# Performance work log

Measured on AMD Instinct MI355X. Metric: run time of the kernel, lower is better.

Reference implementation:

```python
import jax, jax.numpy as jnp
import numpy as np

LEAK = 0.2

def setup_inputs() -> dict:
    key = jax.random.key(0)
    ks = jax.random.split(key, 8)
    B, D, H1, H2, F = 2048, 3072, 512, 256, 100
    s = lambda fan_in: 1.0 / np.sqrt(fan_in)
    return {
        "x":  jax.random.normal(ks[0], (B, D), dtype=jnp.float32),
        "W1": jax.random.uniform(ks[1], (D, H1), jnp.float32, -s(D), s(D)),
        "b1": jnp.zeros((H1,), jnp.float32),
        "W2": jax.random.uniform(ks[2], (H1, H2), jnp.float32, -s(H1), s(H1)),
        "b2": jnp.zeros((H2,), jnp.float32),
        "T":  jax.random.normal(ks[3], (H2, F), dtype=jnp.float32),
        "Wf": jax.random.uniform(ks[4], (H2 + F, 1), jnp.float32, -s(H2 + F), s(H2 + F)),
        "bf": jnp.zeros((1,), jnp.float32),
    }

def reference(x, W1, b1, W2, b2, T, Wf, bf):
    # MLP stack with LeakyReLU(0.2)
    h = jax.nn.leaky_relu(x @ W1 + b1, LEAK)          # (B,512)
    h = jax.nn.leaky_relu(h @ W2 + b2, LEAK)          # (B,256)
    # Minibatch discrimination: pairwise L1 per feature, exp, sum over batch
    m = h @ T                                          # (B,100)
    d = jnp.abs(m[:, None, :] - m[None, :, :])         # (B,B,100)
    feats = jnp.sum(jnp.exp(-d), axis=1)               # (B,100)
    z = jnp.concatenate([h, feats], axis=1)            # (B,356)
    return z @ Wf + bf                                 # (B,1)
```

## Files before the change

### kernel.cpp

```cpp
#include <hip/hip_runtime.h>
#include <hip/hip_bf16.h>

#define LEAK 0.2f

typedef __attribute__((ext_vector_type(8))) short short8;
typedef __attribute__((ext_vector_type(4))) float f32x4;


__global__ __launch_bounds__(256) void k_prep(const float* __restrict__ x,
                                              __hip_bfloat16* __restrict__ xb,
                                              const float* __restrict__ W1,
                                              __hip_bfloat16* __restrict__ W1t,
                                              const float* __restrict__ W2,
                                              __hip_bfloat16* __restrict__ W2t,
                                              const float* __restrict__ T,
                                              __hip_bfloat16* __restrict__ Tt) {
  int b = blockIdx.x;
  int t = threadIdx.x;
  if (b < 6144) {
    int idx = b * 256 + t;
    float4 v = reinterpret_cast<const float4*>(x)[idx];
    union { ushort4 u; __hip_bfloat16 h[4]; } c;
    c.h[0] = __float2bfloat16(v.x);
    c.h[1] = __float2bfloat16(v.y);
    c.h[2] = __float2bfloat16(v.z);
    c.h[3] = __float2bfloat16(v.w);
    reinterpret_cast<ushort4*>(xb)[idx] = c.u;
    return;
  }
  __shared__ float tile[32][33];
  const float* W;
  __hip_bfloat16* Wt;
  int K, N, kblk, nblk;
  int b2 = b - 6144;
  if (b2 < 1536) {
    W = W1; Wt = W1t; K = 3072; N = 512;
    kblk = b2 % 96; nblk = b2 / 96;
  } else if (b2 < 1664) {
    int b3 = b2 - 1536;
    W = W2; Wt = W2t; K = 512; N = 256;
    kblk = b3 % 16; nblk = b3 / 16;
  } else {
    int b4 = b2 - 1664;
    W = T; Wt = Tt; K = 256; N = 100;
    kblk = b4 % 8; nblk = b4 / 8;
  }
  int k0 = kblk * 32, n0 = nblk * 32;
  int tx = t & 31, ty = t >> 5;
#pragma unroll
  for (int r = 0; r < 4; ++r) {
    int n = n0 + tx;
    tile[ty + r * 8][tx] = (n < N) ? W[(long)(k0 + ty + r * 8) * N + n] : 0.f;
  }
  __syncthreads();
#pragma unroll
  for (int r = 0; r < 4; ++r)
    Wt[(long)(n0 + ty + r * 8) * K + k0 + tx] = __float2bfloat16(tile[tx][ty + r * 8]);
}

template <bool TRANSP, bool BF16OUT>
__global__ __launch_bounds__(256) void k_gemm(const __hip_bfloat16* __restrict__ A,
                                              const __hip_bfloat16* __restrict__ Bt,
                                              float* __restrict__ Cp,
                                              int M, int N, int K, int KSPL, int ldO) {
  __shared__ __align__(16) __hip_bfloat16 As[64][72];
  __shared__ __align__(16) __hip_bfloat16 Bs[64][72];
  int tid = threadIdx.x;
  int lane = tid & 63;
  int wv = tid >> 6;
  int wm = wv & 1, wn = wv >> 1;
  int quad = lane >> 4, l16 = lane & 15;
  long m0 = (long)blockIdx.x * 64, n0 = (long)blockIdx.y * 64;
  int srow = tid >> 2, scol = (tid & 3) * 16;
  int kStart = blockIdx.z * KSPL;
  const __hip_bfloat16* Ag = A + (m0 + srow) * K + kStart + scol;
  const __hip_bfloat16* Bg = Bt + (n0 + srow) * K + kStart + scol;

  int4 ra0 = *reinterpret_cast<const int4*>(Ag);
  int4 ra1 = *reinterpret_cast<const int4*>(Ag + 8);
  int4 rb0 = *reinterpret_cast<const int4*>(Bg);
  int4 rb1 = *reinterpret_cast<const int4*>(Bg + 8);

  f32x4 acc[2][2] = {};
  for (int kb = 0; kb < KSPL; kb += 64) {
    *reinterpret_cast<int4*>(&As[srow][scol]) = ra0;
    *reinterpret_cast<int4*>(&As[srow][scol + 8]) = ra1;
    *reinterpret_cast<int4*>(&Bs[srow][scol]) = rb0;
    *reinterpret_cast<int4*>(&Bs[srow][scol + 8]) = rb1;
    __syncthreads();
    if (kb + 64 < KSPL) {
      ra0 = *reinterpret_cast<const int4*>(Ag + kb + 64);
      ra1 = *reinterpret_cast<const int4*>(Ag + kb + 72);
      rb0 = *reinterpret_cast<const int4*>(Bg + kb + 64);
      rb1 = *reinterpret_cast<const int4*>(Bg + kb + 72);
    }
#pragma unroll
    for (int half = 0; half < 2; ++half) {
      short8 af[2], bfr[2];
#pragma unroll
      for (int t = 0; t < 2; ++t) {
        af[t]  = *reinterpret_cast<const short8*>(&As[wm * 32 + t * 16 + l16][half * 32 + quad * 8]);
        bfr[t] = *reinterpret_cast<const short8*>(&Bs[wn * 32 + t * 16 + l16][half * 32 + quad * 8]);
      }
#pragma unroll
      for (int tm = 0; tm < 2; ++tm)
#pragma unroll
        for (int tn = 0; tn < 2; ++tn)
          acc[tm][tn] =
              __builtin_amdgcn_mfma_f32_16x16x32_bf16(af[tm], bfr[tn], acc[tm][tn], 0, 0, 0);
    }
    __syncthreads();
  }

#pragma unroll
  for (int tm = 0; tm < 2; ++tm)
#pragma unroll
    for (int tn = 0; tn < 2; ++tn)
#pragma unroll
      for (int r = 0; r < 4; ++r) {
        long gm = m0 + wm * 32 + tm * 16 + quad * 4 + r;
        long gn = n0 + wn * 32 + tn * 16 + l16;
        long off = TRANSP ? (gn * ldO + gm) : (gm * ldO + gn);
        if constexpr (BF16OUT) {
          __hip_bfloat16* Cz = reinterpret_cast<__hip_bfloat16*>(Cp) + (long)blockIdx.z * M * N;
          Cz[off] = __float2bfloat16(acc[tm][tn][r]);
        } else {
          float* Cz = Cp + (long)blockIdx.z * M * N;
          Cz[off] = acc[tm][tn][r];
        }
      }
}

template <int NZ>
__global__ __launch_bounds__(256) void k_comb_bf(const __hip_bfloat16* __restrict__ P,
                                                 const float* __restrict__ bias,
                                                 __hip_bfloat16* __restrict__ Ob,
                                                 int total8, int nmask) {
  int idx = blockIdx.x * 256 + threadIdx.x;
  if (idx >= total8) return;
  union u8 { short8 v; ushort u[8]; };
  u8 z[NZ], o;
#pragma unroll
  for (int q = 0; q < NZ; ++q)
    z[q].v = reinterpret_cast<const short8*>(P + (long)q * total8 * 8)[idx];
  int col = (idx * 8) & nmask;
  float4 b0 = *reinterpret_cast<const float4*>(bias + col);
  float4 b1 = *reinterpret_cast<const float4*>(bias + col + 4);
  float bs[8] = {b0.x, b0.y, b0.z, b0.w, b1.x, b1.y, b1.z, b1.w};
#pragma unroll
  for (int j = 0; j < 8; ++j) {
    float v = bs[j];
#pragma unroll
    for (int q = 0; q < NZ; ++q) {
      union { ushort u; __hip_bfloat16 h; } cc;
      cc.u = z[q].u[j];
      v += __bfloat162float(cc.h);
    }
    v = v > 0.f ? v : LEAK * v;
    union { ushort u; __hip_bfloat16 h; } co;
    co.h = __float2bfloat16(v);
    o.u[j] = co.u;
  }
  reinterpret_cast<short8*>(Ob)[idx] = o.v;
}

__global__ __launch_bounds__(256) void k_comb2row(const float* __restrict__ P,
                                                  const float* __restrict__ bias,
                                                  const float* __restrict__ Wf,
                                                  const float* __restrict__ bfp,
                                                  __hip_bfloat16* __restrict__ h2b,
                                                  float* __restrict__ out) {
  int wv = threadIdx.x >> 6, lane = threadIdx.x & 63;
  long i = (long)blockIdx.x * 4 + wv;
  long off = i * 256 + lane * 4;
  float4 v = *reinterpret_cast<const float4*>(P + off);
  float4 a = *reinterpret_cast<const float4*>(P + 2048L * 256 + off);
  v.x += a.x; v.y += a.y; v.z += a.z; v.w += a.w;
  float4 bs = *reinterpret_cast<const float4*>(bias + lane * 4);
  v.x += bs.x; v.y += bs.y; v.z += bs.z; v.w += bs.w;
  v.x = v.x > 0.f ? v.x : LEAK * v.x;
  v.y = v.y > 0.f ? v.y : LEAK * v.y;
  v.z = v.z > 0.f ? v.z : LEAK * v.z;
  v.w = v.w > 0.f ? v.w : LEAK * v.w;
  union { ushort4 u; __hip_bfloat16 h[4]; } c;
  c.h[0] = __float2bfloat16(v.x);
  c.h[1] = __float2bfloat16(v.y);
  c.h[2] = __float2bfloat16(v.z);
  c.h[3] = __float2bfloat16(v.w);
  reinterpret_cast<ushort4*>(h2b)[i * 64 + lane] = c.u;
  float4 wfv = *reinterpret_cast<const float4*>(Wf + lane * 4);
  float s = v.x * wfv.x + v.y * wfv.y + v.z * wfv.z + v.w * wfv.w;
#pragma unroll
  for (int d = 32; d; d >>= 1) s += __shfl_down(s, d);
  if (lane == 0) out[i] = s + bfp[0];
}

__global__ __launch_bounds__(1024) void k_bucketfeats(const float* __restrict__ mTz,
                                                      float* __restrict__ featsT) {
  __shared__ float sP[2048], sN[2048];
  __shared__ float Sp[2048], Sn[2048];
  __shared__ int Smeta[2048];
  __shared__ short sB[2048];
  __shared__ int cnt[256], bstart[256], bcur[256];
  __shared__ float bsP[256], bsN[256], Pbel[256], Nab[256];
  __shared__ float wred[32];
  __shared__ float sMin, sMax;
  int f = blockIdx.x;
  int t = threadIdx.x;
  int lane = t & 63, wv = t >> 6;
  const long FS = 2048L * 128;
  const float* row = mTz + (long)f * 2048;

  float m[2];
  float lmin = 3.4e38f, lmax = -3.4e38f;
#pragma unroll
  for (int r = 0; r < 2; ++r) {
    int e = t + r * 1024;
    float v = row[e] + row[FS + e] + row[2 * FS + e] + row[3 * FS + e];
    m[r] = v;
    lmin = fminf(lmin, v);
    lmax = fmaxf(lmax, v);
  }
#pragma unroll
  for (int d = 32; d; d >>= 1) {
    lmin = fminf(lmin, __shfl_down(lmin, d));
    lmax = fmaxf(lmax, __shfl_down(lmax, d));
  }
  if (lane == 0) { wred[wv] = lmin; wred[16 + wv] = lmax; }
  if (t < 256) cnt[t] = 0;
  __syncthreads();
  if (t == 0) {
    float a = wred[0], b = wred[16];
    for (int i = 1; i < 16; ++i) { a = fminf(a, wred[i]); b = fmaxf(b, wred[16 + i]); }
    sMin = a; sMax = b;
  }
  __syncthreads();
  float mn = sMin, mx = sMax;
  float rge = mx - mn;
  float scale = (rge > 1e-20f) ? 255.0f / rge : 0.f;
  float mid = 0.5f * (mn + mx);
#pragma unroll
  for (int r = 0; r < 2; ++r) {
    int e = t + r * 1024;
    float v = m[r];
    int b = (int)((v - mn) * scale);
    b = b < 255 ? b : 255;
    float arg = fminf(fmaxf(v - mid, -60.f), 60.f);
    sP[e] = __expf(arg);
    sN[e] = __expf(-arg);
    sB[e] = (short)b;
    atomicAdd(&cnt[b], 1);
  }
  __syncthreads();
  if (wv == 0) {
    int b4 = lane * 4;
    int c0 = cnt[b4], c1 = cnt[b4 + 1], c2 = cnt[b4 + 2], c3 = cnt[b4 + 3];
    int tot = c0 + c1 + c2 + c3;
    int inc = tot;
#pragma unroll
    for (int d = 1; d < 64; d <<= 1) {
      int y = __shfl_up(inc, d);
      if (lane >= d) inc += y;
    }
    int run = inc - tot;
    bstart[b4] = run; bcur[b4] = run; run += c0;
    bstart[b4 + 1] = run; bcur[b4 + 1] = run; run += c1;
    bstart[b4 + 2] = run; bcur[b4 + 2] = run; run += c2;
    bstart[b4 + 3] = run; bcur[b4 + 3] = run;
  }
  __syncthreads();
#pragma unroll
  for (int r = 0; r < 2; ++r) {
    int e = t + r * 1024;
    int b = sB[e];
    int slot = atomicAdd(&bcur[b], 1);
    Sp[slot] = sP[e];
    Sn[slot] = sN[e];
    Smeta[slot] = (b << 16) | e;
  }
  __syncthreads();
  if (t < 256) {
    int s0 = bstart[t], s1 = s0 + cnt[t];
    float ap = 0.f, an = 0.f;
    for (int q = s0; q < s1; ++q) { ap += Sp[q]; an += Sn[q]; }
    bsP[t] = ap; bsN[t] = an;
  }
  __syncthreads();
  if (wv == 0) {
    int b4 = lane * 4;
    float p0 = bsP[b4], p1 = bsP[b4 + 1], p2 = bsP[b4 + 2], p3 = bsP[b4 + 3];
    float n0 = bsN[b4], n1 = bsN[b4 + 1], n2 = bsN[b4 + 2], n3 = bsN[b4 + 3];
    float tp = p0 + p1 + p2 + p3, tn = n0 + n1 + n2 + n3;
    float ip = tp, in_ = tn;
#pragma unroll
    for (int d = 1; d < 64; d <<= 1) {
      float yp = __shfl_up(ip, d);
      float yn = __shfl_up(in_, d);
      if (lane >= d) { ip += yp; in_ += yn; }
    }
    float totn = __shfl(in_, 63);
    float runp = ip - tp;
    float runn = in_ - tn;
    Pbel[b4] = runp; Nab[b4] = totn - runn - n0; runp += p0; runn += n0;
    Pbel[b4 + 1] = runp; Nab[b4 + 1] = totn - runn - n1; runp += p1; runn += n1;
    Pbel[b4 + 2] = runp; Nab[b4 + 2] = totn - runn - n2; runp += p2; runn += n2;
    Pbel[b4 + 3] = runp; Nab[b4 + 3] = totn - runn - n3;
  }
  __syncthreads();
#pragma unroll
  for (int r = 0; r < 2; ++r) {
    int s = t + r * 1024;
    int meta = Smeta[s];
    int b = meta >> 16;
    int idx = meta & 0xFFFF;
    float p = Sp[s], n = Sn[s];
    float acc = n * Pbel[b] + p * Nab[b];
    int q0 = bstart[b], q1 = q0 + cnt[b];
    for (int q = q0; q < q1; ++q) acc += fminf(p * Sn[q], n * Sp[q]);
    featsT[(long)f * 2048 + idx] = acc;
  }
}

__global__ __launch_bounds__(256) void k_final(const float* __restrict__ featsT,
                                               const float* __restrict__ Wf,
                                               float* __restrict__ out) {
  int wv = threadIdx.x >> 6, lane = threadIdx.x & 63;
  long i = (long)blockIdx.x * 4 + wv;
  float s = 0.f;
  for (int f = lane; f < 100; f += 64) s += featsT[(long)f * 2048 + i] * Wf[256 + f];
#pragma unroll
  for (int off = 32; off; off >>= 1) s += __shfl_down(s, off);
  if (lane == 0) out[i] += s;
}

extern "C" void kernel_launch(void* const* d_in, const int* in_sizes, int n_in,
                              void* d_out, int out_size, void* d_ws, size_t ws_size,
                              hipStream_t stream) {
  const float* x  = (const float*)d_in[0];
  const float* W1 = (const float*)d_in[1];
  const float* b1 = (const float*)d_in[2];
  const float* W2 = (const float*)d_in[3];
  const float* b2 = (const float*)d_in[4];
  const float* T  = (const float*)d_in[5];
  const float* Wf = (const float*)d_in[6];
  const float* bf = (const float*)d_in[7];
  float* out = (float*)d_out;

  char* w = (char*)d_ws;
  auto alloc = [&](size_t b) { char* p = w; w += (b + 255) & ~(size_t)255; return p; };
  __hip_bfloat16* xb  = (__hip_bfloat16*)alloc(2048L * 3072 * 2);
  __hip_bfloat16* W1t = (__hip_bfloat16*)alloc(512L * 3072 * 2);
  __hip_bfloat16* W2t = (__hip_bfloat16*)alloc(256L * 512 * 2);
  __hip_bfloat16* Tt  = (__hip_bfloat16*)alloc(128L * 256 * 2);
  __hip_bfloat16* h1b = (__hip_bfloat16*)alloc(2048L * 512 * 2);
  __hip_bfloat16* h2b = (__hip_bfloat16*)alloc(2048L * 256 * 2);
  float*          feT = (float*)alloc(100L * 2048 * 4);
  __hip_bfloat16* P1  = (__hip_bfloat16*)alloc(6L * 2048 * 512 * 2);
  float*          P2  = (float*)alloc(2L * 2048 * 256 * 4);
  float*          P3  = (float*)alloc(4L * 2048 * 128 * 4);

  k_prep<<<7840, 256, 0, stream>>>(x, xb, W1, W1t, W2, W2t, T, Tt);
  k_gemm<false, true><<<dim3(32, 8, 6), 256, 0, stream>>>(xb, W1t, (float*)P1, 2048, 512, 3072, 512, 512);
  k_comb_bf<6><<<512, 256, 0, stream>>>(P1, b1, h1b, 131072, 511);
  k_gemm<false, false><<<dim3(32, 4, 2), 256, 0, stream>>>(h1b, W2t, P2, 2048, 256, 512, 256, 256);
  k_comb2row<<<512, 256, 0, stream>>>(P2, b2, Wf, bf, h2b, out);
  k_gemm<true, false><<<dim3(32, 2, 4), 256, 0, stream>>>(h2b, Tt, P3, 2048, 128, 256, 64, 2048);
  k_bucketfeats<<<100, 1024, 0, stream>>>(P3, feT);
  k_final<<<512, 256, 0, stream>>>(feT, Wf, out);
}
```

Before: 126.9 us.

## Stage transposed GEMM output through LDS, halve split-K, use bf16 partials for layer 2

The transposed-output GEMM now writes its tile to shared memory and stores coalesced float4 rows, replacing scattered strided writes. The first GEMM's split-K count drops from six to three slices, which halves the partial-sum traffic and the reduction work in the combine kernel but leaves fewer blocks to run in parallel. The second GEMM now writes bf16 partials instead of fp32, and the combine kernel reads bf16, trading some accuracy for less memory traffic.

```diff
diff --git a/kernel.cpp b/kernel.cpp
--- a/kernel.cpp
+++ b/kernel.cpp
@@ -63,6 +63,7 @@
                                               const __hip_bfloat16* __restrict__ Bt,
                                               float* __restrict__ Cp,
                                               int M, int N, int K, int KSPL, int ldO) {
+  static_assert(!(TRANSP && BF16OUT), "unused combo");
   __shared__ __align__(16) __hip_bfloat16 As[64][72];
   __shared__ __align__(16) __hip_bfloat16 Bs[64][72];
   int tid = threadIdx.x;
@@ -112,23 +113,46 @@
     __syncthreads();
   }
 
-#pragma unroll
-  for (int tm = 0; tm < 2; ++tm)
-#pragma unroll
-    for (int tn = 0; tn < 2; ++tn)
-#pragma unroll
-      for (int r = 0; r < 4; ++r) {
-        long gm = m0 + wm * 32 + tm * 16 + quad * 4 + r;
-        long gn = n0 + wn * 32 + tn * 16 + l16;
-        long off = TRANSP ? (gn * ldO + gm) : (gm * ldO + gn);
-        if constexpr (BF16OUT) {
-          __hip_bfloat16* Cz = reinterpret_cast<__hip_bfloat16*>(Cp) + (long)blockIdx.z * M * N;
-          Cz[off] = __float2bfloat16(acc[tm][tn][r]);
-        } else {
-          float* Cz = Cp + (long)blockIdx.z * M * N;
-          Cz[off] = acc[tm][tn][r];
+  if constexpr (TRANSP) {
+    __shared__ float Sf[64][65];
+#pragma unroll
+    for (int tm = 0; tm < 2; ++tm)
+#pragma unroll
+      for (int tn = 0; tn < 2; ++tn)
+#pragma unroll
+        for (int r = 0; r < 4; ++r) {
+          int lr = wm * 32 + tm * 16 + quad * 4 + r;
+          int lc = wn * 32 + tn * 16 + l16;
+          Sf[lc][lr] = acc[tm][tn][r];
         }
-      }
+    __syncthreads();
+    float* Cz = Cp + (long)blockIdx.z * M * N;
+#pragma unroll
+    for (int p = 0; p < 4; ++p) {
+      int idx = p * 256 + tid;
+      int row = idx >> 4, cc = (idx & 15) * 4;
+      float4 v = *reinterpret_cast<const float4*>(&Sf[row][cc]);
+      *reinterpret_cast<float4*>(Cz + (n0 + row) * ldO + m0 + cc) = v;
+    }
+  } else {
+#pragma unroll
+    for (int tm = 0; tm < 2; ++tm)
+#pragma unroll
+      for (int tn = 0; tn < 2; ++tn)
+#pragma unroll
+        for (int r = 0; r < 4; ++r) {
+          long gm = m0 + wm * 32 + tm * 16 + quad * 4 + r;
+          long gn = n0 + wn * 32 + tn * 16 + l16;
+          long off = gm * ldO + gn;
+          if constexpr (BF16OUT) {
+            __hip_bfloat16* Cz = reinterpret_cast<__hip_bfloat16*>(Cp) + (long)blockIdx.z * M * N;
+            Cz[off] = __float2bfloat16(acc[tm][tn][r]);
+          } else {
+            float* Cz = Cp + (long)blockIdx.z * M * N;
+            Cz[off] = acc[tm][tn][r];
+          }
+        }
+  }
 }
 
 template <int NZ>
@@ -164,7 +188,7 @@
   reinterpret_cast<short8*>(Ob)[idx] = o.v;
 }
 
-__global__ __launch_bounds__(256) void k_comb2row(const float* __restrict__ P,
+__global__ __launch_bounds__(256) void k_comb2row(const __hip_bfloat16* __restrict__ P,
                                                   const float* __restrict__ bias,
                                                   const float* __restrict__ Wf,
                                                   const float* __restrict__ bfp,
@@ -172,10 +196,17 @@
                                                   float* __restrict__ out) {
   int wv = threadIdx.x >> 6, lane = threadIdx.x & 63;
   long i = (long)blockIdx.x * 4 + wv;
-  long off = i * 256 + lane * 4;
-  float4 v = *reinterpret_cast<const float4*>(P + off);
-  float4 a = *reinterpret_cast<const float4*>(P + 2048L * 256 + off);
-  v.x += a.x; v.y += a.y; v.z += a.z; v.w += a.w;
+  long off4 = i * 64 + lane;
+  ushort4 pa = reinterpret_cast<const ushort4*>(P)[off4];
+  ushort4 pb = reinterpret_cast<const ushort4*>(P + 2048L * 256)[off4];
+  union { ushort u; __hip_bfloat16 h; } c0, c1, c2, c3, d0, d1, d2, d3;
+  c0.u = pa.x; c1.u = pa.y; c2.u = pa.z; c3.u = pa.w;
+  d0.u = pb.x; d1.u = pb.y; d2.u = pb.z; d3.u = pb.w;
+  float4 v;
+  v.x = __bfloat162float(c0.h) + __bfloat162float(d0.h);
+  v.y = __bfloat162float(c1.h) + __bfloat162float(d1.h);
+  v.z = __bfloat162float(c2.h) + __bfloat162float(d2.h);
+  v.w = __bfloat162float(c3.h) + __bfloat162float(d3.h);
   float4 bs = *reinterpret_cast<const float4*>(bias + lane * 4);
   v.x += bs.x; v.y += bs.y; v.z += bs.z; v.w += bs.w;
   v.x = v.x > 0.f ? v.x : LEAK * v.x;
@@ -355,14 +386,14 @@
   __hip_bfloat16* h1b = (__hip_bfloat16*)alloc(2048L * 512 * 2);
   __hip_bfloat16* h2b = (__hip_bfloat16*)alloc(2048L * 256 * 2);
   float*          feT = (float*)alloc(100L * 2048 * 4);
-  __hip_bfloat16* P1  = (__hip_bfloat16*)alloc(6L * 2048 * 512 * 2);
-  float*          P2  = (float*)alloc(2L * 2048 * 256 * 4);
+  __hip_bfloat16* P1  = (__hip_bfloat16*)alloc(3L * 2048 * 512 * 2);
+  __hip_bfloat16* P2  = (__hip_bfloat16*)alloc(2L * 2048 * 256 * 2);
   float*          P3  = (float*)alloc(4L * 2048 * 128 * 4);
 
   k_prep<<<7840, 256, 0, stream>>>(x, xb, W1, W1t, W2, W2t, T, Tt);
-  k_gemm<false, true><<<dim3(32, 8, 6), 256, 0, stream>>>(xb, W1t, (float*)P1, 2048, 512, 3072, 512, 512);
-  k_comb_bf<6><<<512, 256, 0, stream>>>(P1, b1, h1b, 131072, 511);
-  k_gemm<false, false><<<dim3(32, 4, 2), 256, 0, stream>>>(h1b, W2t, P2, 2048, 256, 512, 256, 256);
+  k_gemm<false, true><<<dim3(32, 8, 3), 256, 0, stream>>>(xb, W1t, (float*)P1, 2048, 512, 3072, 1024, 512);
+  k_comb_bf<3><<<512, 256, 0, stream>>>(P1, b1, h1b, 131072, 511);
+  k_gemm<false, true><<<dim3(32, 4, 2), 256, 0, stream>>>(h1b, W2t, (float*)P2, 2048, 256, 512, 256, 256);
   k_comb2row<<<512, 256, 0, stream>>>(P2, b2, Wf, bf, h2b, out);
   k_gemm<true, false><<<dim3(32, 2, 4), 256, 0, stream>>>(h2b, Tt, P3, 2048, 128, 256, 64, 2048);
   k_bucketfeats<<<100, 1024, 0, stream>>>(P3, feT);
```

Result: no change. 127.9 us (+0.7%).
